# Performance work log

Measured on AMD Instinct MI355X. Metric: run time of the kernel, lower is better.

## Reference

```python
import jax, jax.numpy as jnp
import numpy as np

EMBED = 1024
HEADS = 16
HEAD_DIM = EMBED // HEADS
CAUSAL = True
NUM_SEQS = 8
SEQ = 1024
TOTAL = NUM_SEQS * SEQ


def setup_inputs() -> dict:
    key = jax.random.key(0)
    ks = jax.random.split(key, 8)
    s = 0.02
    return {
        "hidden_states": jax.random.normal(ks[0], (TOTAL, EMBED), dtype=jnp.float32),
        "seq_len": jnp.full((NUM_SEQS,), SEQ, dtype=jnp.int64),
        "Wq": jax.random.normal(ks[1], (EMBED, EMBED), dtype=jnp.float32) * s,
        "bq": jnp.zeros((EMBED,), dtype=jnp.float32),
        "Wk": jax.random.normal(ks[2], (EMBED, EMBED), dtype=jnp.float32) * s,
        "Wv": jax.random.normal(ks[3], (EMBED, EMBED), dtype=jnp.float32) * s,
        "bv": jnp.zeros((EMBED,), dtype=jnp.float32),
        "Wo": jax.random.normal(ks[4], (EMBED, EMBED), dtype=jnp.float32) * s,
        "bo": jnp.zeros((EMBED,), dtype=jnp.float32),
    }


def _varlen_attention(q, k, v, seq_len):
    # q,k,v: [T, H, D] packed ragged tokens; seq_len: static per-sequence lengths.
    # Equivalent to the per-sequence Python loop, but done as one padded batch.
    sl = np.asarray(seq_len)
    B = sl.shape[0]
    S = int(sl.max())
    cu = np.concatenate([[0], np.cumsum(sl)])  # cu_seqlens
    pos = np.arange(S)
    # gather indices [B, S] (clipped inside each segment; invalid masked below)
    idx = cu[:-1, None] + np.minimum(pos[None, :], sl[:, None] - 1)
    valid = pos[None, :] < sl[:, None]  # [B, S]
    qp, kp, vp = q[idx], k[idx], v[idx]  # [B, S, H, D]
    scale = 1.0 / np.float32(np.sqrt(q.shape[-1]))
    scores = jnp.einsum('bqhd,bkhd->bhqk', qp, kp) * scale  # [B, H, S, S]
    mask = valid[:, None, None, :]  # valid keys
    if CAUSAL:
        mask = mask & (pos[None, :] <= pos[:, None])[None, None, :, :]
    scores = jnp.where(mask, scores, -jnp.inf)
    probs = jax.nn.softmax(scores, axis=-1)
    out = jnp.einsum('bhqk,bkhd->bqhd', probs, vp)  # [B, S, H, D]
    # unpad back to packed layout [T, H*D]
    b_of = np.repeat(np.arange(B), sl)
    p_of = np.concatenate([np.arange(l) for l in sl])
    return out[b_of, p_of].reshape(q.shape[0], -1)


def reference(hidden_states, seq_len, Wq, bq, Wk, Wv, bv, Wo, bo):
    T = hidden_states.shape[0]
    q = (hidden_states @ Wq.T + bq).reshape(T, HEADS, HEAD_DIM)
    k = (hidden_states @ Wk.T).reshape(T, HEADS, HEAD_DIM)  # k_proj has no bias
    v = (hidden_states @ Wv.T + bv).reshape(T, HEADS, HEAD_DIM)
    attn = _varlen_attention(q, k, v, seq_len)  # [T, EMBED]
    return attn @ Wo.T + bo
```

## Files before the change

### kernel.cpp

```cpp
#include <hip/hip_runtime.h>
#include <hip/hip_bf16.h>


typedef unsigned short u16;
typedef unsigned int   u32;
typedef __attribute__((ext_vector_type(8))) short bf16x8;
typedef __attribute__((ext_vector_type(4))) float f32x4;
typedef __attribute__((ext_vector_type(16))) float f32x16;
typedef __attribute__((ext_vector_type(4))) u32 u32x4;

#define AS1 __attribute__((address_space(1)))
#define AS3 __attribute__((address_space(3)))

__device__ __forceinline__ u16 f2bf(float f) {
  u32 x = __float_as_uint(f);
  x += 0x7fffu + ((x >> 16) & 1u);
  return (u16)(x >> 16);
}
__device__ __forceinline__ u32 pk2(float a, float b) {
  return (u32)f2bf(a) | ((u32)f2bf(b) << 16);
}

__global__ __launch_bounds__(256) void cvt_all(const float* __restrict__ hs,
                                               const float* __restrict__ Wq,
                                               const float* __restrict__ Wk,
                                               const float* __restrict__ Wv,
                                               const float* __restrict__ Wo,
                                               u16* __restrict__ Xb,
                                               u16* __restrict__ Wqkv,
                                               u16* __restrict__ Wob) {
  int i = blockIdx.x * 256 + threadIdx.x;
  const int stride = gridDim.x * 256;
  for (; i < 3145728; i += stride) {
    const float* src;
    u16* dst;
    int off;
    if (i < 2097152) {
      src = hs; dst = Xb; off = i;
    } else {
      int j = i - 2097152;
      int m = j >> 18;
      off = j & 262143;
      src = (m == 0) ? Wq : (m == 1) ? Wk : (m == 2) ? Wv : Wo;
      dst = (m < 3) ? (Wqkv + (size_t)m * 1048576) : Wob;
    }
    float4 v = ((const float4*)src)[off];
    u32 lo = (u32)f2bf(v.x) | ((u32)f2bf(v.y) << 16);
    u32 hi = (u32)f2bf(v.z) | ((u32)f2bf(v.w) << 16);
    ((u32*)dst)[off * 2]     = lo;
    ((u32*)dst)[off * 2 + 1] = hi;
  }
}

__global__ __launch_bounds__(256) void build_bias(const float* __restrict__ bq,
                                                  const float* __restrict__ bv,
                                                  float* __restrict__ bias) {
  int i = blockIdx.x * blockDim.x + threadIdx.x;
  if (i >= 3072) return;
  float v = 0.f;
  if (i < 1024) v = bq[i];
  else if (i >= 2048) v = bv[i - 2048];
  bias[i] = v;
}

template <int OUT_MODE>
__global__ __launch_bounds__(256) void gemm_nt(const u16* __restrict__ A,
                                               const u16* __restrict__ Bw,
                                               const float* __restrict__ bias,
                                               void* __restrict__ C,
                                               int M, int N, int K, int nbn) {
  __shared__ __align__(16) u16 As[128 * 32];
  __shared__ __align__(16) u16 Bs[128 * 32];
  const int cpx = gridDim.x >> 3;
  const int swz = (blockIdx.x & 7) * cpx + (blockIdx.x >> 3);
  const int bn = swz % nbn, bm = swz / nbn;
  const int tid = threadIdx.x;
  const int l = tid & 63, w = tid >> 6;
  const int l15 = l & 15, lg = l >> 4;
  const int wr = w >> 1, wc = w & 1;

  f32x4 acc[4][4] = {};

  const u16* Ab = A + (size_t)(bm * 128) * K;
  const u16* Bb = Bw + (size_t)(bn * 128) * K;

  const int srow = w * 16 + (l >> 2);
  const int sk = (l & 3) * 8;

  for (int k0 = 0; k0 < K; k0 += 32) {
#pragma unroll
    for (int i = 0; i < 2; ++i) {
      int row = i * 64 + srow;
      __builtin_amdgcn_global_load_lds(
          (const AS1 void*)(Ab + (size_t)row * K + k0 + sk),
          (AS3 void*)((AS3 u16*)As + i * 2048 + w * 512), 16, 0, 0);
      __builtin_amdgcn_global_load_lds(
          (const AS1 void*)(Bb + (size_t)row * K + k0 + sk),
          (AS3 void*)((AS3 u16*)Bs + i * 2048 + w * 512), 16, 0, 0);
    }
    __syncthreads();
    bf16x8 af[4], bf[4];
#pragma unroll
    for (int m = 0; m < 4; ++m)
      af[m] = *(const bf16x8*)&As[(wr * 64 + m * 16 + l15) * 32 + lg * 8];
#pragma unroll
    for (int n = 0; n < 4; ++n)
      bf[n] = *(const bf16x8*)&Bs[(wc * 64 + n * 16 + l15) * 32 + lg * 8];
#pragma unroll
    for (int m = 0; m < 4; ++m)
#pragma unroll
      for (int n = 0; n < 4; ++n)
        acc[m][n] = __builtin_amdgcn_mfma_f32_16x16x32_bf16(af[m], bf[n], acc[m][n], 0, 0, 0);
    __syncthreads();
  }

#pragma unroll
  for (int m = 0; m < 4; ++m) {
#pragma unroll
    for (int i = 0; i < 4; ++i) {
      int row = bm * 128 + wr * 64 + m * 16 + lg * 4 + i;
#pragma unroll
      for (int n = 0; n < 4; ++n) {
        int col = bn * 128 + wc * 64 + n * 16 + l15;
        float v = acc[m][n][i] + bias[col];
        if (OUT_MODE == 0)
          ((u16*)C)[(size_t)row * N + col] = f2bf(v);
        else
          ((float*)C)[(size_t)row * N + col] = v;
      }
    }
  }
}

__global__ __launch_bounds__(256, 4) void attn_kernel(const u16* __restrict__ qkv,
                                                      u16* __restrict__ attnout) {
  const int bid = (blockIdx.x & 7) * 128 + (blockIdx.x >> 3);
  const int qb = 7 - (bid & 7);
  const int h = (bid >> 3) & 15;
  const int s = bid >> 7;
  const int tid = threadIdx.x;
  const int l = tid & 63, w = tid >> 6;
  const int l31 = l & 31;
  const int hi = l >> 5;
  const int pb = (l >> 3) & 1;

  __shared__ __align__(16) u16 Ks[128 * 64];
  __shared__ __align__(16) u32 Vt2[64 * 65];

  const u16* kbase = qkv + (size_t)(s * 1024) * 3072 + 1024 + h * 64;
  const u16* vbase = qkv + (size_t)(s * 1024) * 3072 + 2048 + h * 64;

  bf16x8 qf[4];
  {
    const u16* qptr = qkv + (size_t)(s * 1024 + qb * 128 + w * 32 + l31) * 3072 + h * 64 + hi * 8;
#pragma unroll
    for (int c = 0; c < 4; ++c) qf[c] = *(const bf16x8*)(qptr + c * 16);
  }

  float m_r = -1e30f, l_r = 0.f;
  f32x16 o0 = {}, o1 = {};

  const int nt = qb + 1;

  const int vkv = w * 8 + (l >> 3);
  const int vd0 = (l & 7) * 8;
  const int vkp = w * 4 + (l >> 4);
  const int dEff = vd0 + pb * 4;

  const int srow = w * 8 + (l >> 3);
  const int schunk = (l & 7) ^ ((l >> 3) & 7);

  bf16x8 vcur[4], vnx[4];
#pragma unroll
  for (int p = 0; p < 4; ++p)
    vcur[p] = *(const bf16x8*)(vbase + (size_t)(p * 32 + vkv) * 3072 + vd0);

  for (int t = 0; t < nt; ++t) {
    const u16* kt = kbase + (size_t)(t * 128) * 3072;
#pragma unroll
    for (int p = 0; p < 4; ++p)
      __builtin_amdgcn_global_load_lds(
          (const AS1 void*)(kt + (size_t)(p * 32 + srow) * 3072 + schunk * 8),
          (AS3 void*)((AS3 u16*)Ks + p * 2048 + w * 512), 16, 0, 0);

#pragma unroll
    for (int p = 0; p < 4; ++p) {
      u32 dw0 = ((u32*)&vcur[p])[0], dw1 = ((u32*)&vcur[p])[1];
      u32 dw2 = ((u32*)&vcur[p])[2], dw3 = ((u32*)&vcur[p])[3];
      u32 s0 = (u32)__shfl_xor((int)(pb ? dw0 : dw2), 8, 64);
      u32 s1 = (u32)__shfl_xor((int)(pb ? dw1 : dw3), 8, 64);
      u32 md0 = pb ? dw2 : dw0, md1 = pb ? dw3 : dw1;
      u32 lo0 = pb ? s0 : md0, hi0 = pb ? md0 : s0;
      u32 lo1 = pb ? s1 : md1, hi1 = pb ? md1 : s1;
      int kp = p * 16 + vkp;
      Vt2[(dEff + 0) * 65 + kp] = (lo0 & 0xffffu) | (hi0 << 16);
      Vt2[(dEff + 1) * 65 + kp] = (lo0 >> 16) | (hi0 & 0xffff0000u);
      Vt2[(dEff + 2) * 65 + kp] = (lo1 & 0xffffu) | (hi1 << 16);
      Vt2[(dEff + 3) * 65 + kp] = (lo1 >> 16) | (hi1 & 0xffff0000u);
    }
    __syncthreads();

    if (t + 1 < nt) {
      const u16* vt = vbase + (size_t)((t + 1) * 128) * 3072;
#pragma unroll
      for (int p = 0; p < 4; ++p)
        vnx[p] = *(const bf16x8*)(vt + (size_t)(p * 32 + vkv) * 3072 + vd0);
    }

    const bool diag = (t == nt - 1);
#pragma unroll
    for (int sub = 0; sub < 4; ++sub) {
      if (!(diag && sub > w)) {
        f32x16 sc = {};
#pragma unroll
        for (int c = 0; c < 4; ++c) {
          int r = sub * 32 + l31;
          int pc = (2 * c + hi) ^ (l31 & 7);
          bf16x8 kf = *(const bf16x8*)&Ks[r * 64 + pc * 8];
          sc = __builtin_amdgcn_mfma_f32_32x32x16_bf16(kf, qf[c], sc, 0, 0, 0);
        }
        float tv[16];
#pragma unroll
        for (int r = 0; r < 16; ++r) tv[r] = sc[r] * 0.125f;
        if (diag && sub == w) {
#pragma unroll
          for (int r = 0; r < 16; ++r) {
            int kvloc = (r & 3) + 8 * (r >> 2) + 4 * hi;
            if (kvloc > l31) tv[r] = -1e30f;
          }
        }
        float t0 = fmaxf(fmaxf(tv[0], tv[1]), fmaxf(tv[2], tv[3]));
        float t1 = fmaxf(fmaxf(tv[4], tv[5]), fmaxf(tv[6], tv[7]));
        float t2 = fmaxf(fmaxf(tv[8], tv[9]), fmaxf(tv[10], tv[11]));
        float t3 = fmaxf(fmaxf(tv[12], tv[13]), fmaxf(tv[14], tv[15]));
        float tmax = fmaxf(fmaxf(t0, t1), fmaxf(t2, t3));
        tmax = fmaxf(tmax, __shfl_xor(tmax, 32, 64));
        if (!__all(tmax <= m_r + 8.0f)) {
          float nm = fmaxf(m_r, tmax);
          float alpha = __expf(m_r - nm);
          m_r = nm;
          l_r *= alpha;
#pragma unroll
          for (int r = 0; r < 16; ++r) { o0[r] *= alpha; o1[r] *= alpha; }
        }
#pragma unroll
        for (int r = 0; r < 16; ++r) tv[r] = __expf(tv[r] - m_r);
        float s0_ = (tv[0] + tv[1]) + (tv[2] + tv[3]);
        float s1_ = (tv[4] + tv[5]) + (tv[6] + tv[7]);
        float s2_ = (tv[8] + tv[9]) + (tv[10] + tv[11]);
        float s3_ = (tv[12] + tv[13]) + (tv[14] + tv[15]);
        float psum = (s0_ + s1_) + (s2_ + s3_);
        psum += __shfl_xor(psum, 32, 64);
        l_r += psum;
#pragma unroll
        for (int s01 = 0; s01 < 2; ++s01) {
          u32 W0 = pk2(tv[8 * s01 + 0], tv[8 * s01 + 1]);
          u32 W1 = pk2(tv[8 * s01 + 2], tv[8 * s01 + 3]);
          u32 X0 = pk2(tv[8 * s01 + 4], tv[8 * s01 + 5]);
          u32 X1 = pk2(tv[8 * s01 + 6], tv[8 * s01 + 7]);
          u32 rW0 = (u32)__shfl_xor((int)W0, 32, 64);
          u32 rW1 = (u32)__shfl_xor((int)W1, 32, 64);
          u32 rX0 = (u32)__shfl_xor((int)X0, 32, 64);
          u32 rX1 = (u32)__shfl_xor((int)X1, 32, 64);
          u32x4 av;
          av[0] = hi ? rX0 : W0;
          av[1] = hi ? rX1 : W1;
          av[2] = hi ? X0 : rW0;
          av[3] = hi ? X1 : rW1;
          bf16x8 pa = *(bf16x8*)&av;
          int kpb = sub * 16 + s01 * 8 + hi * 4;
          u32x4 v0 = *(const u32x4*)&Vt2[(size_t)l31 * 65 + kpb];
          o0 = __builtin_amdgcn_mfma_f32_32x32x16_bf16(pa, *(bf16x8*)&v0, o0, 0, 0, 0);
          u32x4 v1 = *(const u32x4*)&Vt2[(size_t)(32 + l31) * 65 + kpb];
          o1 = __builtin_amdgcn_mfma_f32_32x32x16_bf16(pa, *(bf16x8*)&v1, o1, 0, 0, 0);
        }
      }
    }
    __syncthreads();
#pragma unroll
    for (int p = 0; p < 4; ++p) vcur[p] = vnx[p];
  }

#pragma unroll
  for (int r = 0; r < 16; ++r) {
    int qp = (r & 3) + 8 * (r >> 2) + 4 * hi;
    float ls = __shfl(l_r, qp, 64);
    float inv = __builtin_amdgcn_rcpf(ls);
    int trow = s * 1024 + qb * 128 + w * 32 + qp;
    attnout[(size_t)trow * 1024 + h * 64 + l31]      = f2bf(o0[r] * inv);
    attnout[(size_t)trow * 1024 + h * 64 + 32 + l31] = f2bf(o1[r] * inv);
  }
}

extern "C" void kernel_launch(void* const* d_in, const int* in_sizes, int n_in,
                              void* d_out, int out_size, void* d_ws, size_t ws_size,
                              hipStream_t stream) {
  const float* hs = (const float*)d_in[0];
  const float* Wq = (const float*)d_in[2];
  const float* bq = (const float*)d_in[3];
  const float* Wk = (const float*)d_in[4];
  const float* Wv = (const float*)d_in[5];
  const float* bv = (const float*)d_in[6];
  const float* Wo = (const float*)d_in[7];
  const float* bo = (const float*)d_in[8];

  char* ws = (char*)d_ws;
  u16* Xb    = (u16*)ws;
  u16* Wqkv  = (u16*)(ws + 16777216);
  u16* Wob   = (u16*)(ws + 23068672);
  float* bqk = (float*)(ws + 25165824);
  u16* qkv   = (u16*)(ws + 25178112);
  u16* attn  = (u16*)(ws + 75509760);

  cvt_all<<<2048, 256, 0, stream>>>(hs, Wq, Wk, Wv, Wo, Xb, Wqkv, Wob);
  build_bias<<<12, 256, 0, stream>>>(bq, bv, bqk);

  gemm_nt<0><<<1536, 256, 0, stream>>>(Xb, Wqkv, bqk, qkv, 8192, 3072, 1024, 24);

  attn_kernel<<<1024, 256, 0, stream>>>(qkv, attn);

  gemm_nt<1><<<512, 256, 0, stream>>>(attn, Wob, bo, d_out, 8192, 1024, 1024, 8);
}
```

Before: 287.0 us.

## Replace GEMM with 256x256 double-buffered 8-wave pipelined kernel; fold bias build into convert

Replaces the 128x128 single-buffered GEMM with a 256x256-tile, 512-thread kernel. It double-buffers A and B in XOR-swizzled LDS, interleaves global-to-LDS staging with four MFMA quadrants per k-step, and raises wave priority around the MFMA blocks. The aim is to hide load latency, reduce LDS bank conflicts and increase operand reuse per tile. The separate bias-building kernel is merged into the conversion kernel to save one launch. The cost is far fewer blocks: 128 for the output projection on a many-CU GPU, which risks poor occupancy, along with much more LDS use per block and complex manual vmcnt/barrier synchronisation.

```diff
diff --git a/kernel.cpp b/kernel.cpp
--- a/kernel.cpp
+++ b/kernel.cpp
@@ -11,6 +11,8 @@
 
 #define AS1 __attribute__((address_space(1)))
 #define AS3 __attribute__((address_space(3)))
+#define FENCE asm volatile("" ::: "memory")
+#define BAR() do { FENCE; __builtin_amdgcn_s_barrier(); FENCE; } while (0)
 
 __device__ __forceinline__ u16 f2bf(float f) {
   u32 x = __float_as_uint(f);
@@ -26,9 +28,20 @@
                                                const float* __restrict__ Wk,
                                                const float* __restrict__ Wv,
                                                const float* __restrict__ Wo,
+                                               const float* __restrict__ bq,
+                                               const float* __restrict__ bv,
                                                u16* __restrict__ Xb,
                                                u16* __restrict__ Wqkv,
-                                               u16* __restrict__ Wob) {
+                                               u16* __restrict__ Wob,
+                                               float* __restrict__ bias) {
+  if (blockIdx.x == gridDim.x - 1) {
+    for (int i = threadIdx.x; i < 3072; i += 256) {
+      float v = 0.f;
+      if (i < 1024) v = bq[i];
+      else if (i >= 2048) v = bv[i - 2048];
+      bias[i] = v;
+    }
+  }
   int i = blockIdx.x * 256 + threadIdx.x;
   const int stride = gridDim.x * 256;
   for (; i < 3145728; i += stride) {
@@ -52,84 +65,147 @@
   }
 }
 
-__global__ __launch_bounds__(256) void build_bias(const float* __restrict__ bq,
-                                                  const float* __restrict__ bv,
-                                                  float* __restrict__ bias) {
-  int i = blockIdx.x * blockDim.x + threadIdx.x;
-  if (i >= 3072) return;
-  float v = 0.f;
-  if (i < 1024) v = bq[i];
-  else if (i >= 2048) v = bv[i - 2048];
-  bias[i] = v;
+__device__ __forceinline__ void quad16(f32x4 (&acc)[4][2],
+                                       const bf16x8 (&af)[4][2],
+                                       const bf16x8 (&bf)[2][2]) {
+#pragma unroll
+  for (int m = 0; m < 4; ++m)
+#pragma unroll
+    for (int n = 0; n < 2; ++n)
+#pragma unroll
+      for (int kk = 0; kk < 2; ++kk)
+        acc[m][n] = __builtin_amdgcn_mfma_f32_16x16x32_bf16(
+            af[m][kk], bf[n][kk], acc[m][n], 0, 0, 0);
 }
 
 template <int OUT_MODE>
-__global__ __launch_bounds__(256) void gemm_nt(const u16* __restrict__ A,
-                                               const u16* __restrict__ Bw,
-                                               const float* __restrict__ bias,
-                                               void* __restrict__ C,
-                                               int M, int N, int K, int nbn) {
-  __shared__ __align__(16) u16 As[128 * 32];
-  __shared__ __align__(16) u16 Bs[128 * 32];
+__global__ __launch_bounds__(512, 2) void gemm8p(const u16* __restrict__ A,
+                                                 const u16* __restrict__ Bw,
+                                                 const float* __restrict__ bias,
+                                                 void* __restrict__ C,
+                                                 int M, int N, int K, int nbn) {
+  __shared__ __align__(16) u16 sA[2][2][128 * 64];
+  __shared__ __align__(16) u16 sB[2][2][128 * 64];
+
   const int cpx = gridDim.x >> 3;
-  const int swz = (blockIdx.x & 7) * cpx + (blockIdx.x >> 3);
+  const int swz = ((int)blockIdx.x & 7) * cpx + ((int)blockIdx.x >> 3);
   const int bn = swz % nbn, bm = swz / nbn;
   const int tid = threadIdx.x;
   const int l = tid & 63, w = tid >> 6;
-  const int l15 = l & 15, lg = l >> 4;
-  const int wr = w >> 1, wc = w & 1;
-
-  f32x4 acc[4][4] = {};
-
-  const u16* Ab = A + (size_t)(bm * 128) * K;
-  const u16* Bb = Bw + (size_t)(bn * 128) * K;
-
-  const int srow = w * 16 + (l >> 2);
-  const int sk = (l & 3) * 8;
-
-  for (int k0 = 0; k0 < K; k0 += 32) {
-#pragma unroll
-    for (int i = 0; i < 2; ++i) {
-      int row = i * 64 + srow;
+  const int l15 = l & 15, lg = (l >> 4) & 3;
+  const int wr = w >> 2, wc = w & 3;
+  const int bh = wc >> 1;
+
+  const u16* Ab = A + (size_t)(bm * 256) * K;
+  const u16* Bb = Bw + (size_t)(bn * 256) * K;
+
+  const int sr = w * 8 + (l >> 3);
+  const int sch = (l & 7) ^ ((l >> 3) & 7);
+  const int sldso = w * 64 * 8;
+
+  auto STAGE = [&](const u16* Xb, u16* lds, int hf, int kt) {
+    const u16* src = Xb + (size_t)(hf * 128) * K + kt * 64;
+#pragma unroll
+    for (int j = 0; j < 2; ++j)
       __builtin_amdgcn_global_load_lds(
-          (const AS1 void*)(Ab + (size_t)row * K + k0 + sk),
-          (AS3 void*)((AS3 u16*)As + i * 2048 + w * 512), 16, 0, 0);
-      __builtin_amdgcn_global_load_lds(
-          (const AS1 void*)(Bb + (size_t)row * K + k0 + sk),
-          (AS3 void*)((AS3 u16*)Bs + i * 2048 + w * 512), 16, 0, 0);
-    }
-    __syncthreads();
-    bf16x8 af[4], bf[4];
+          (const AS1 void*)(src + (size_t)(j * 64 + sr) * K + sch * 8),
+          (AS3 void*)((AS3 u16*)lds + j * 512 * 8 + sldso), 16, 0, 0);
+  };
+  auto LDA = [&](const u16* Ah, int mh, int m, int kk) -> bf16x8 {
+    int row = mh * 64 + m * 16 + l15;
+    int ch = (kk * 4 + lg) ^ (l15 & 7);
+    return *(const bf16x8*)&Ah[row * 64 + ch * 8];
+  };
+  auto LDB = [&](const u16* Bh, int nh, int n, int kk) -> bf16x8 {
+    int row = (wc & 1) * 64 + nh * 32 + n * 16 + l15;
+    int ch = (kk * 4 + lg) ^ (l15 & 7);
+    return *(const bf16x8*)&Bh[row * 64 + ch * 8];
+  };
+
+  f32x4 acc[2][2][4][2] = {};
+  const int NT = K >> 6;
+
+  STAGE(Ab, &sA[0][0][0], 0, 0);
+  STAGE(Ab, &sA[0][1][0], 1, 0);
+  STAGE(Bb, &sB[0][0][0], 0, 0);
+  STAGE(Bb, &sB[0][1][0], 1, 0);
+  STAGE(Bb, &sB[1][0][0], 0, 1);
+  STAGE(Bb, &sB[1][1][0], 1, 1);
+  asm volatile("s_waitcnt vmcnt(4)" ::: "memory");
+  BAR();
+
+  for (int kt = 0; kt < NT; ++kt) {
+    const int p = kt & 1;
+    const u16* Ah = &sA[p][wr][0];
+    const u16* Bh = &sB[p][bh][0];
+    bf16x8 af0[4][2], af1[4][2], bf0[2][2], bf1[2][2];
+
 #pragma unroll
     for (int m = 0; m < 4; ++m)
-      af[m] = *(const bf16x8*)&As[(wr * 64 + m * 16 + l15) * 32 + lg * 8];
-#pragma unroll
-    for (int n = 0; n < 4; ++n)
-      bf[n] = *(const bf16x8*)&Bs[(wc * 64 + n * 16 + l15) * 32 + lg * 8];
+#pragma unroll
+      for (int kk = 0; kk < 2; ++kk) af0[m][kk] = LDA(Ah, 0, m, kk);
+#pragma unroll
+    for (int n = 0; n < 2; ++n)
+#pragma unroll
+      for (int kk = 0; kk < 2; ++kk) bf0[n][kk] = LDB(Bh, 0, n, kk);
+    if (kt + 1 < NT) STAGE(Ab, &sA[p ^ 1][0][0], 0, kt + 1);
+    BAR();
+    __builtin_amdgcn_s_setprio(1);
+    quad16(acc[0][0], af0, bf0);
+    __builtin_amdgcn_s_setprio(0);
+    BAR();
+
+#pragma unroll
+    for (int n = 0; n < 2; ++n)
+#pragma unroll
+      for (int kk = 0; kk < 2; ++kk) bf1[n][kk] = LDB(Bh, 1, n, kk);
+    if (kt + 1 < NT) STAGE(Ab, &sA[p ^ 1][1][0], 1, kt + 1);
+    BAR();
+    __builtin_amdgcn_s_setprio(1);
+    quad16(acc[0][1], af0, bf1);
+    __builtin_amdgcn_s_setprio(0);
+    BAR();
+
 #pragma unroll
     for (int m = 0; m < 4; ++m)
 #pragma unroll
-      for (int n = 0; n < 4; ++n)
-        acc[m][n] = __builtin_amdgcn_mfma_f32_16x16x32_bf16(af[m], bf[n], acc[m][n], 0, 0, 0);
-    __syncthreads();
-  }
-
-#pragma unroll
-  for (int m = 0; m < 4; ++m) {
-#pragma unroll
-    for (int i = 0; i < 4; ++i) {
-      int row = bm * 128 + wr * 64 + m * 16 + lg * 4 + i;
-#pragma unroll
-      for (int n = 0; n < 4; ++n) {
-        int col = bn * 128 + wc * 64 + n * 16 + l15;
-        float v = acc[m][n][i] + bias[col];
-        if (OUT_MODE == 0)
-          ((u16*)C)[(size_t)row * N + col] = f2bf(v);
-        else
-          ((float*)C)[(size_t)row * N + col] = v;
+      for (int kk = 0; kk < 2; ++kk) af1[m][kk] = LDA(Ah, 1, m, kk);
+    if (kt + 2 < NT) STAGE(Bb, &sB[p][0][0], 0, kt + 2);
+    BAR();
+    __builtin_amdgcn_s_setprio(1);
+    quad16(acc[1][1], af1, bf1);
+    __builtin_amdgcn_s_setprio(0);
+    BAR();
+
+    if (kt + 2 < NT) STAGE(Bb, &sB[p][1][0], 1, kt + 2);
+    BAR();
+    __builtin_amdgcn_s_setprio(1);
+    quad16(acc[1][0], af1, bf0);
+    __builtin_amdgcn_s_setprio(0);
+    if (kt >= NT - 2) asm volatile("s_waitcnt vmcnt(0)" ::: "memory");
+    else              asm volatile("s_waitcnt vmcnt(4)" ::: "memory");
+    BAR();
+  }
+
+#pragma unroll
+  for (int mh = 0; mh < 2; ++mh)
+#pragma unroll
+    for (int m = 0; m < 4; ++m)
+#pragma unroll
+      for (int i = 0; i < 4; ++i) {
+        int row = bm * 256 + wr * 128 + mh * 64 + m * 16 + lg * 4 + i;
+#pragma unroll
+        for (int nh = 0; nh < 2; ++nh)
+#pragma unroll
+          for (int n = 0; n < 2; ++n) {
+            int col = bn * 256 + wc * 64 + nh * 32 + n * 16 + l15;
+            float v = acc[mh][nh][m][n][i] + bias[col];
+            if (OUT_MODE == 0)
+              ((u16*)C)[(size_t)row * N + col] = f2bf(v);
+            else
+              ((float*)C)[(size_t)row * N + col] = v;
+          }
       }
-    }
-  }
 }
 
 __global__ __launch_bounds__(256, 4) void attn_kernel(const u16* __restrict__ qkv,
@@ -312,12 +388,11 @@
   u16* qkv   = (u16*)(ws + 25178112);
   u16* attn  = (u16*)(ws + 75509760);
 
-  cvt_all<<<2048, 256, 0, stream>>>(hs, Wq, Wk, Wv, Wo, Xb, Wqkv, Wob);
-  build_bias<<<12, 256, 0, stream>>>(bq, bv, bqk);
-
-  gemm_nt<0><<<1536, 256, 0, stream>>>(Xb, Wqkv, bqk, qkv, 8192, 3072, 1024, 24);
+  cvt_all<<<2048, 256, 0, stream>>>(hs, Wq, Wk, Wv, Wo, bq, bv, Xb, Wqkv, Wob, bqk);
+
+  gemm8p<0><<<384, 512, 0, stream>>>(Xb, Wqkv, bqk, qkv, 8192, 3072, 1024, 12);
 
   attn_kernel<<<1024, 256, 0, stream>>>(qkv, attn);
 
-  gemm_nt<1><<<512, 256, 0, stream>>>(attn, Wob, bo, d_out, 8192, 1024, 1024, 8);
-}
+  gemm8p<1><<<128, 512, 0, stream>>>(attn, Wob, bo, d_out, 8192, 1024, 1024, 4);
+}
```

Measured after the change: 264.0 us. 8.0% less time.
